# Kernel optimization log

Measured on AMD Instinct MI355X. Metric: run time of the kernel, lower is better.

## Reference

```python
import jax, jax.numpy as jnp
import numpy as np

B, L, D = 4, 2048, 768
K, M, CK = 12, 1, 4            # heads, thetas, conv kernel size
H = D // (K * M)               # 64
DIM_MEM = K * H                # 768
DIM_EXPAND = H * 3             # 192
DSH = DIM_EXPAND * 2           # 384 swiglu head dim
DST = K * DSH                  # 4608
DIM_FUSED = DIM_MEM + K + DST  # 5388
THETA_MIN, THETA_MAX = 1e-3, 3.0


def setup_inputs() -> dict:
    key = jax.random.key(0)
    ks = jax.random.split(key, 5)
    x = jax.random.normal(ks[0], (B, L, D), jnp.float32)
    W_in = jax.random.normal(ks[1], (D, DIM_FUSED), jnp.float32) * 0.02
    conv_w = jax.random.normal(ks[2], (CK, DIM_MEM + K), jnp.float32) * 0.2  # depthwise taps
    rms_scale = jnp.ones((H,), jnp.float32)
    # theta_raw init (M==1 branch): inverse-sigmoid of geomspace grid
    grid = np.geomspace(THETA_MIN, THETA_MAX, K).reshape(1, 1, K, 1, 1)
    base = np.tile(grid, (1, 1, 1, H, 1))
    u = np.clip((base - THETA_MIN) / (THETA_MAX - THETA_MIN), 1e-4, 1 - 1e-4)
    theta_raw = jnp.asarray(np.log(u) - np.log(1.0 - u), jnp.float32)
    decay_slopes = jnp.asarray(np.log(np.exp(np.geomspace(1e-3, 0.1, K)) - 1.0), jnp.float32)
    score_scale = jnp.ones((K,), jnp.float32)
    tanh_scale = jnp.ones((K,), jnp.float32)
    W_sw = jax.random.normal(ks[3], (2 * K * H * M, DST), jnp.float32) * 0.02
    W_out = jax.random.normal(ks[4], (K * DIM_EXPAND, D), jnp.float32) * 0.02
    return {"x": x, "W_in": W_in, "conv_w": conv_w, "rms_scale": rms_scale,
            "theta_raw": theta_raw, "decay_slopes": decay_slopes,
            "score_scale": score_scale, "tanh_scale": tanh_scale,
            "W_sw": W_sw, "W_out": W_out}


def reference(x, W_in, conv_w, rms_scale, theta_raw, decay_slopes,
              score_scale, tanh_scale, W_sw, W_out):
    # fused in-projection
    z_fused = jnp.einsum('bld,df->blf', x, W_in)
    z_mem = z_fused[..., :DIM_MEM + K]
    skip_direct = z_fused[..., DIM_MEM + K:]
    # causal depthwise conv (kernel size CK, left pad CK-1)
    zp = jnp.pad(z_mem, ((0, 0), (CK - 1, 0), (0, 0)))
    z_conv = sum(zp[:, j:j + L, :] * conv_w[j] for j in range(CK))
    z_mem = jax.nn.silu(z_conv)
    # memory keys + RMSNorm over H
    k_val = z_mem[..., :DIM_MEM].reshape(B, L, K, H)
    k_val = k_val * jax.lax.rsqrt(jnp.mean(k_val * k_val, axis=-1, keepdims=True) + 1e-6) * rms_scale
    s_raw = z_mem[..., DIM_MEM:]  # (B, L, K)
    # theta (M == 1)
    theta = THETA_MIN + (THETA_MAX - THETA_MIN) * jax.nn.sigmoid(theta_raw)  # (1,1,K,H,1)
    # decay time weights (num_anchor_heads == 0, maxlen == L)
    pos = jnp.arange(L, dtype=jnp.float32)
    slopes = jax.nn.softplus(decay_slopes).reshape(1, 1, K)
    dist = jnp.maximum(jnp.float32(L - 1) - pos, 0.0)
    log_time_weight = -slopes * dist[None, :, None]  # (1, L, K)
    log_p = jnp.clip(score_scale[None, None, :] * s_raw, -10.0, 10.0)
    p_w = jnp.exp(log_p + log_time_weight)  # (B, L, K)
    # characteristic-function encoding
    k5 = k_val[..., None]  # (B, L, K, H, 1)
    phi = jnp.tanh(k5 * tanh_scale.reshape(1, 1, K, 1, 1)) * theta
    kvw = k5 * p_w[..., None, None]
    re = kvw * jnp.cos(phi)
    im = kvw * jnp.sin(phi)
    # fused causal cumulative accumulation
    flat = K * H * M
    stack = jnp.concatenate([p_w, re.reshape(B, L, flat), im.reshape(B, L, flat)], axis=-1)
    cs = jnp.cumsum(stack, axis=1)
    den_acc = cs[..., :K]
    re_acc = cs[..., K:K + flat].reshape(B, L, K, H, M)
    im_acc = cs[..., K + flat:].reshape(B, L, K, H, M)
    inv_den = (1.0 / jnp.maximum(den_acc, 1e-4))[..., None, None]
    summary_flat = jnp.stack([re_acc * inv_den, im_acc * inv_den], axis=-1).reshape(B, L, -1)
    # SwiGLU with skip
    y_spectral = jnp.einsum('bls,sf->blf', summary_flat, W_sw).reshape(B, L, K, DSH)
    y_skip = skip_direct.reshape(B, L, K, DSH)
    y_spec_val, y_spec_gate = jnp.split(y_spectral, 2, axis=-1)
    y_skip_val, y_skip_gate = jnp.split(y_skip, 2, axis=-1)
    y_act = (y_spec_val + y_skip_val) * jax.nn.silu(y_spec_gate + y_skip_gate)
    out = jnp.einsum('blf,fd->bld', y_act.reshape(B, L, -1), W_out)
    return out
```

## Files before the change

### kernel.cpp

```cpp
#include <hip/hip_runtime.h>
#include <hip/hip_bf16.h>

#define B_       4
#define L_       2048
#define D_       768
#define K_       12
#define H_       64
#define CK_      4
#define DIM_MEM_ 768
#define DMK      780
#define NT       (B_*L_)
#define NSUM     1536
#define NACT     2304
#define NCHUNK   16
#define CHLEN    (L_/NCHUNK)
#define PSTRIDE  132

typedef __attribute__((ext_vector_type(8))) short          bf16x8;
typedef __attribute__((ext_vector_type(8))) unsigned short u16x8;
typedef __attribute__((ext_vector_type(4))) float          f32x4;

__device__ __forceinline__ ushort f2bf(float v) {
    __hip_bfloat16 h = __float2bfloat16(v);
    return *reinterpret_cast<ushort*>(&h);
}
__device__ __forceinline__ float tanh_fast(float x) {
    float t = __expf(-2.f * fabsf(x));
    float r = (1.f - t) / (1.f + t);
    return copysignf(r, x);
}

struct PrepJobs {
    const float* W[6];
    ushort*      out[6];
    int ldw[6], Kd[6], colbase[6], remap[6], ntx[6];
    int start[7];
    const float* cast_in;
    ushort*      cast_out;
    int n4;
};

__global__ __launch_bounds__(256)
void prep_all(PrepJobs J)
{
    int blk = blockIdx.x;
    if (blk >= J.start[6]) {
        int i = (blk - J.start[6]) * 256 + threadIdx.x;
        if (i < J.n4) {
            float4 v = reinterpret_cast<const float4*>(J.cast_in)[i];
            ushort4 o;
            o.x = f2bf(v.x); o.y = f2bf(v.y); o.z = f2bf(v.z); o.w = f2bf(v.w);
            reinterpret_cast<ushort4*>(J.cast_out)[i] = o;
        }
        return;
    }
    int j = 0;
    while (blk >= J.start[j + 1]) ++j;
    int rel = blk - J.start[j];
    int ntx = J.ntx[j];
    int n0 = (rel % ntx) * 32, k0 = (rel / ntx) * 32;
    const float* W = J.W[j];
    int ldw = J.ldw[j], Kd = J.Kd[j], colbase = J.colbase[j], remap = J.remap[j];
    ushort* out = J.out[j];

    __shared__ float tile[32][33];
    int tx = threadIdx.x & 31, ty = threadIdx.x >> 5;
    int n = n0 + tx;
    int c;
    if (remap) {
        int grp = n >> 5, which = (n >> 4) & 1, nn = (grp << 4) + (n & 15);
        c = colbase + (nn / 192) * 384 + which * 192 + (nn % 192);
    } else {
        c = colbase + n;
    }
    #pragma unroll
    for (int r = 0; r < 4; ++r)
        tile[ty + r*8][tx] = W[(size_t)(k0 + ty + r*8) * ldw + c];
    __syncthreads();
    #pragma unroll
    for (int r = 0; r < 4; ++r)
        out[(size_t)(n0 + ty + r*8) * Kd + k0 + tx] = f2bf(tile[tx][ty + r*8]);
}

__global__ __launch_bounds__(256)
void gemm_bf16_mfma(const ushort* __restrict__ A, const ushort* __restrict__ BT,
                    float* __restrict__ C, int Kd, int N, int ldc)
{
    __shared__ ushort As[128*64];
    __shared__ ushort Bs[128*64];
    int tid = threadIdx.x, lane = tid & 63;
    int lr = lane & 15, quad = lane >> 4;
    int wave = tid >> 6;
    int wr = (wave >> 1) * 64, wc = (wave & 1) * 64;
    int m0 = blockIdx.y * 128, n0 = blockIdx.x * 128;

    f32x4 acc[4][4] = {};

    int srow = tid >> 3;
    int tc   = tid & 7;
    const ushort* gA = A  + (size_t)(m0 + srow) * Kd + tc * 8;
    const ushort* gB = BT + (size_t)(n0 + srow) * Kd + tc * 8;
    int woff = srow * 64 + ((tc ^ (srow & 7)) * 8);
    int rx = lr & 7;

    for (int k0 = 0; k0 < Kd; k0 += 64) {
        u16x8 a[4], b[4];
        #pragma unroll
        for (int p = 0; p < 4; ++p) {
            a[p] = *reinterpret_cast<const u16x8*>(gA + (size_t)(32*p) * Kd);
            b[p] = *reinterpret_cast<const u16x8*>(gB + (size_t)(32*p) * Kd);
        }
        gA += 64; gB += 64;
        __syncthreads();
        #pragma unroll
        for (int p = 0; p < 4; ++p) {
            *reinterpret_cast<u16x8*>(As + woff + p*2048) = a[p];
            *reinterpret_cast<u16x8*>(Bs + woff + p*2048) = b[p];
        }
        __syncthreads();
        #pragma unroll
        for (int ks = 0; ks < 2; ++ks) {
            bf16x8 af[4], bf[4];
            #pragma unroll
            for (int i = 0; i < 4; ++i) {
                int ca = ((ks*4 + quad) ^ rx) * 8;
                af[i] = *reinterpret_cast<const bf16x8*>(As + (wr + i*16 + lr) * 64 + ca);
                bf[i] = *reinterpret_cast<const bf16x8*>(Bs + (wc + i*16 + lr) * 64 + ca);
            }
            #pragma unroll
            for (int i = 0; i < 4; ++i)
                #pragma unroll
                for (int j = 0; j < 4; ++j)
                    acc[i][j] = __builtin_amdgcn_mfma_f32_16x16x32_bf16(
                                    af[i], bf[j], acc[i][j], 0, 0, 0);
        }
    }

    #pragma unroll
    for (int i = 0; i < 4; ++i)
        #pragma unroll
        for (int j = 0; j < 4; ++j)
            #pragma unroll
            for (int r = 0; r < 4; ++r) {
                int row = m0 + wr + i*16 + quad*4 + r;
                int col = n0 + wc + j*16 + lr;
                if (col < N)
                    C[(size_t)row * ldc + col] = acc[i][j][r];
            }
}

#define G2NKT 36

#define GLOAD16(gp, dp) __builtin_amdgcn_global_load_lds( \
    (__attribute__((address_space(1))) const void*)(gp),  \
    (__attribute__((address_space(3))) void*)(dp), 16, 0, 0)

__device__ __forceinline__ void g2_stageA(ushort* lds_, int kt,
                                          const ushort* pAs, const ushort* pAx,
                                          int wave, int part)
{
    int ktc = kt > (G2NKT-1) ? (G2NKT-1) : kt;
    const ushort* g; size_t kd;
    if (ktc < 24) { g = pAs + ktc*64;      kd = 1536; }
    else          { g = pAx + (ktc-24)*64; kd = 768;  }
    g += (size_t)(part * 64) * kd;
    ushort* d = lds_ + (kt & 1) * 8192 + part * 4096 + wave * 512;
    GLOAD16(g,           d);
    GLOAD16(g + 32*kd,   d + 2048);
}

__device__ __forceinline__ void g2_stageB(ushort* lds_, int kt,
                                          const ushort* pBs, const ushort* pBx,
                                          int wave)
{
    int ktc = kt > (G2NKT-1) ? (G2NKT-1) : kt;
    const ushort* g; size_t kd;
    if (ktc < 24) { g = pBs + ktc*64;      kd = 1536; }
    else          { g = pBx + (ktc-24)*64; kd = 768;  }
    ushort* d = lds_ + 16384 + (kt & 1) * 12288 + wave * 512;
    #pragma unroll
    for (int s = 0; s < 6; ++s)
        GLOAD16(g + (size_t)(32*s)*kd, d + 2048*s);
}

__global__ __launch_bounds__(256, 2)
void gemm2_1ph(const ushort* __restrict__ Sm, const ushort* __restrict__ Xb,
               const ushort* __restrict__ WsC, const ushort* __restrict__ WiC,
               ushort* __restrict__ yact)
{
    __shared__ ushort lds[40960];
    const int tid  = threadIdx.x;
    const int lane = tid & 63, wave = tid >> 6;
    const int lr = lane & 15, quad = lane >> 4, rx = lr & 7;
    const int wr = (wave >> 1) * 64;
    const int wc = (wave & 1) * 96;
    const int m0 = blockIdx.y * 128, n0 = blockIdx.x * 192;

    const int sr = tid >> 3;
    const int sc = (tid & 7) ^ (sr & 7);
    const ushort* pAs = Sm  + (size_t)(m0 + sr) * 1536 + sc * 8;
    const ushort* pAx = Xb  + (size_t)(m0 + sr) * 768  + sc * 8;
    const ushort* pBs = WsC + (size_t)(n0 + sr) * 1536 + sc * 8;
    const ushort* pBx = WiC + (size_t)(n0 + sr) * 768  + sc * 8;

    f32x4 acc[4][6] = {};
    const int ca0 = (quad ^ rx) * 8;
    const int ca1 = ((4 + quad) ^ rx) * 8;

    g2_stageA(lds, 0, pAs, pAx, wave, 0);
    g2_stageA(lds, 0, pAs, pAx, wave, 1);
    g2_stageB(lds, 0, pBs, pBx, wave);
    asm volatile("s_waitcnt vmcnt(0)" ::: "memory");
    __builtin_amdgcn_s_barrier();

    #pragma unroll 1
    for (int g = 0; g < G2NKT; ++g) {
        const ushort* Ab = lds + (g & 1) * 8192;
        const ushort* Bb = lds + 16384 + (g & 1) * 12288;

        g2_stageA(lds, g + 1, pAs, pAx, wave, 0);
        g2_stageA(lds, g + 1, pAs, pAx, wave, 1);
        g2_stageB(lds, g + 1, pBs, pBx, wave);

        bf16x8 af[4][2], bfr[6][2];
        #pragma unroll
        for (int i = 0; i < 4; ++i) {
            const ushort* p = Ab + (wr + i*16 + lr) * 64;
            af[i][0] = *reinterpret_cast<const bf16x8*>(p + ca0);
            af[i][1] = *reinterpret_cast<const bf16x8*>(p + ca1);
        }
        #pragma unroll
        for (int j = 0; j < 6; ++j) {
            const ushort* p = Bb + (wc + j*16 + lr) * 64;
            bfr[j][0] = *reinterpret_cast<const bf16x8*>(p + ca0);
            bfr[j][1] = *reinterpret_cast<const bf16x8*>(p + ca1);
        }
        __builtin_amdgcn_s_setprio(1);
        #pragma unroll
        for (int ks = 0; ks < 2; ++ks)
            #pragma unroll
            for (int i = 0; i < 4; ++i)
                #pragma unroll
                for (int j = 0; j < 6; ++j)
                    acc[i][j] = __builtin_amdgcn_mfma_f32_16x16x32_bf16(
                                    af[i][ks], bfr[j][ks], acc[i][j], 0, 0, 0);
        __builtin_amdgcn_s_setprio(0);

        asm volatile("s_waitcnt vmcnt(0)" ::: "memory");
        __builtin_amdgcn_s_barrier();
    }

    const int vg0 = (n0 + wc) >> 5;
    #pragma unroll
    for (int i = 0; i < 4; ++i)
        #pragma unroll
        for (int p = 0; p < 3; ++p)
            #pragma unroll
            for (int r = 0; r < 4; ++r) {
                int row = m0 + wr + i*16 + quad*4 + r;
                int col = (vg0 + p)*16 + lr;
                float v  = acc[i][2*p][r];
                float gt = acc[i][2*p + 1][r];
                float y = v * (gt / (1.f + __expf(-gt)));
                yact[(size_t)row * NACT + col] = f2bf(y);
            }
}

__global__ __launch_bounds__(128)
void token_scan1(const float* __restrict__ zmem, const float* __restrict__ conv_w,
                 const float* __restrict__ rms_scale, const float* __restrict__ theta_raw,
                 const float* __restrict__ dslopes, const float* __restrict__ sscale,
                 const float* __restrict__ tscale,
                 float* __restrict__ reN, float* __restrict__ imN,
                 float* __restrict__ pwN, float* __restrict__ part)
{
    int blk = blockIdx.x;
    int chunk = blk & (NCHUNK - 1);
    int bk = blk >> 4;
    int k = bk % K_;
    int b = bk / K_;
    int tid = threadIdx.x;
    int h = tid & 63;
    int tt = tid >> 6;
    int l0 = chunk * CHLEN + tt * 64;

    int c  = k*H_ + h;
    int cs = DIM_MEM_ + k;

    float cw0 = conv_w[0*DMK + c], cw1 = conv_w[1*DMK + c];
    float cw2 = conv_w[2*DMK + c], cw3 = conv_w[3*DMK + c];
    float cs0 = conv_w[0*DMK + cs], cs1 = conv_w[1*DMK + cs];
    float cs2 = conv_w[2*DMK + cs], cs3 = conv_w[3*DMK + cs];
    float rs  = rms_scale[h];
    float th  = 0.001f + 2.999f * (1.f / (1.f + __expf(-theta_raw[c])));
    float ts  = tscale[k];
    float scl = sscale[k];
    float slope = log1pf(expf(dslopes[k]));

    const float* zb = zmem + (size_t)(b*L_) * DMK;

    float z3=0.f, z2=0.f, z1=0.f, s3=0.f, s2=0.f, s1=0.f;
    {
        int ll = l0 - 3;
        if (ll >= 0)     { z3 = zb[(size_t)ll*DMK + c];     s3 = zb[(size_t)ll*DMK + cs]; }
        if (ll + 1 >= 0) { z2 = zb[(size_t)(ll+1)*DMK + c]; s2 = zb[(size_t)(ll+1)*DMK + cs]; }
        if (ll + 2 >= 0) { z1 = zb[(size_t)(ll+2)*DMK + c]; s1 = zb[(size_t)(ll+2)*DMK + cs]; }
    }

    float sre = 0.f, sim = 0.f, spw = 0.f;
    size_t obase = (size_t)blk * (CHLEN*H_) + (size_t)(tt*64)*H_ + h;

    for (int i0 = 0; i0 < 64; i0 += 8) {
        float zl[8], sl[8];
        #pragma unroll
        for (int j = 0; j < 8; ++j) {
            int l = l0 + i0 + j;
            zl[j] = zb[(size_t)l*DMK + c];
            sl[j] = zb[(size_t)l*DMK + cs];
        }
        #pragma unroll
        for (int j = 0; j < 8; ++j) {
            int l = l0 + i0 + j;
            float a3 = zl[j], b3 = sl[j];
            float acc  = cw0*z3 + cw1*z2 + cw2*z1 + cw3*a3;
            float acc2 = cs0*s3 + cs1*s2 + cs2*s1 + cs3*b3;
            z3 = z2; z2 = z1; z1 = a3;
            s3 = s2; s2 = s1; s1 = b3;

            float kv = acc / (1.f + __expf(-acc));
            float ss = kv * kv;
            #pragma unroll
            for (int off = 32; off > 0; off >>= 1)
                ss += __shfl_xor(ss, off, 64);
            float kn  = kv * rsqrtf(ss * (1.f/64.f) + 1e-6f) * rs;
            float phi = tanh_fast(kn * ts) * th;

            float s  = acc2 / (1.f + expf(-acc2));
            float lp = fminf(10.f, fmaxf(-10.f, scl * s));
            float pwv = expf(lp - slope * (float)(L_ - 1 - l));

            float kvw = kn * pwv;
            float rev = kvw * __cosf(phi);
            float imv = kvw * __sinf(phi);
            reN[obase + (size_t)(i0 + j)*H_] = rev;
            imN[obase + (size_t)(i0 + j)*H_] = imv;
            sre += rev; sim += imv; spw += pwv;
            if (h == 0) pwN[(size_t)bk * L_ + l] = pwv;
        }
    }

    __shared__ float red[2][64], imd[2][64], pwd[2];
    red[tt][h] = sre; imd[tt][h] = sim;
    if (h == 0) pwd[tt] = spw;
    __syncthreads();
    size_t pb = (size_t)blk * PSTRIDE;
    if (tid < 64) part[pb + tid] = red[0][tid] + red[1][tid];
    else          part[pb + tid] = imd[0][tid - 64] + imd[1][tid - 64];
    if (tid == 0) part[pb + 128] = pwd[0] + pwd[1];
}

__global__ __launch_bounds__(128)
void scan_final2(const float* __restrict__ pwN, const float* __restrict__ reN,
                 const float* __restrict__ imN, const float* __restrict__ part,
                 ushort* __restrict__ summary)
{
    int blk = blockIdx.x;
    int chunk = blk & (NCHUNK - 1);
    int bk = blk >> 4;
    int k = bk % K_;
    int b = bk / K_;
    int tid = threadIdx.x;
    int h = tid & 63;
    int pi = tid >> 6;
    const float* __restrict__ src = pi ? imN : reN;
    int l0 = chunk * CHLEN;

    float acc = 0.f, dacc = 0.f;
    size_t pb0 = (size_t)(bk * NCHUNK) * PSTRIDE;
    for (int cn = 0; cn < chunk; ++cn) {
        acc  += part[pb0 + (size_t)cn*PSTRIDE + tid];
        dacc += part[pb0 + (size_t)cn*PSTRIDE + 128];
    }

    size_t base  = (size_t)blk * (CHLEN*H_) + h;
    size_t dbase = (size_t)bk * L_ + l0;
    int outch = 2*(k*H_ + h) + pi;
    for (int i0 = 0; i0 < CHLEN; i0 += 8) {
        float v[8], d[8];
        #pragma unroll
        for (int j = 0; j < 8; ++j) {
            v[j] = src[base + (size_t)(i0 + j)*H_];
            d[j] = pwN[dbase + i0 + j];
        }
        #pragma unroll
        for (int j = 0; j < 8; ++j) {
            acc += v[j]; dacc += d[j];
            float inv = 1.f / fmaxf(dacc, 1e-4f);
            summary[((size_t)(b*L_ + l0 + i0 + j))*NSUM + outch] = f2bf(acc * inv);
        }
    }
}

extern "C" void kernel_launch(void* const* d_in, const int* in_sizes, int n_in,
                              void* d_out, int out_size, void* d_ws, size_t ws_size,
                              hipStream_t stream)
{
    const float* x         = (const float*)d_in[0];
    const float* W_in      = (const float*)d_in[1];
    const float* conv_w    = (const float*)d_in[2];
    const float* rms_scale = (const float*)d_in[3];
    const float* theta_raw = (const float*)d_in[4];
    const float* dslopes   = (const float*)d_in[5];
    const float* sscale    = (const float*)d_in[6];
    const float* tscale    = (const float*)d_in[7];
    const float* W_sw      = (const float*)d_in[8];
    const float* W_out     = (const float*)d_in[9];
    float* out = (float*)d_out;
    char* ws   = (char*)d_ws;

    float*  zmem    = (float*) (ws + 0);
    ushort* summary = (ushort*)(ws + 0);
    float*  pw      = (float*) (ws + 25559040);
    float*  re      = (float*) (ws + 25952256);
    float*  im      = (float*) (ws + 51118080);
    ushort* yact    = (ushort*)(ws + 25952256);
    float*  part    = (float*) (ws + 76283904);
    ushort* xb      = (ushort*)(ws + 76689408);
    ushort* WiCat   = (ushort*)(ws + 89272320);
    ushort* WsCat   = (ushort*)(ws + 96350208);
    ushort* WoT     = (ushort*)(ws + 110505984);
    ushort* WimT    = (ushort*)(ws + 114044928);

    PrepJobs J{};
    J.W[0]=W_in;  J.out[0]=WiCat; J.ldw[0]=5388; J.Kd[0]=768;  J.colbase[0]=780; J.remap[0]=1; J.ntx[0]=144;
    J.W[1]=W_sw;  J.out[1]=WsCat; J.ldw[1]=4608; J.Kd[1]=1536; J.colbase[1]=0;   J.remap[1]=1; J.ntx[1]=144;
    J.W[2]=W_out; J.out[2]=WoT;   J.ldw[2]=768;  J.Kd[2]=2304; J.colbase[2]=0;   J.remap[2]=0; J.ntx[2]=24;
    J.W[3]=W_in;  J.out[3]=WimT;  J.ldw[3]=5388; J.Kd[3]=768;  J.colbase[3]=0;   J.remap[3]=0; J.ntx[3]=28;
    int tiles[4] = {144*24, 144*48, 24*72, 28*24};
    J.start[0] = 0;
    for (int j = 0; j < 4; ++j) J.start[j+1] = J.start[j] + tiles[j];
    J.start[5] = J.start[4];
    J.start[6] = J.start[4];
    J.cast_in = x; J.cast_out = xb; J.n4 = NT*D_/4;
    int nblk = J.start[6] + (J.n4 + 255)/256;

    dim3 blk(256);
    prep_all<<<dim3(nblk), blk, 0, stream>>>(J);
    gemm_bf16_mfma<<<dim3(7, 64), blk, 0, stream>>>(xb, WimT, zmem, 768, 780, 780);
    token_scan1<<<dim3(B_*K_*NCHUNK), dim3(128), 0, stream>>>(
        zmem, conv_w, rms_scale, theta_raw, dslopes, sscale, tscale,
        re, im, pw, part);
    scan_final2<<<dim3(B_*K_*NCHUNK), dim3(128), 0, stream>>>(pw, re, im, part, summary);
    gemm2_1ph<<<dim3(24, 64), dim3(256), 0, stream>>>(summary, xb, WsCat, WiCat, yact);
    gemm_bf16_mfma<<<dim3(6, 64), blk, 0, stream>>>(yact, WoT, out, 2304, 768, 768);
}
```

Measured before the change: 399.3 us.

## Double-buffer GEMM tiles with direct global-to-LDS loads in first and last GEMMs

Replaces the register-staged single-buffer bf16 MFMA GEMM with a version that uses global_load_lds to copy tiles straight into a double-buffered LDS region. The next K-tile is prefetched while the current one is used, with one barrier per iteration instead of two. All fragments for a tile are loaded up front, and s_setprio raises wave priority around the MFMA block. The kernel doubles its LDS use (64KB) and adds launch bounds for two blocks per CU, which could limit occupancy.

```diff
diff --git a/kernel.cpp b/kernel.cpp
--- a/kernel.cpp
+++ b/kernel.cpp
@@ -82,58 +82,78 @@
         out[(size_t)(n0 + ty + r*8) * Kd + k0 + tx] = f2bf(tile[tx][ty + r*8]);
 }
 
-__global__ __launch_bounds__(256)
-void gemm_bf16_mfma(const ushort* __restrict__ A, const ushort* __restrict__ BT,
-                    float* __restrict__ C, int Kd, int N, int ldc)
-{
-    __shared__ ushort As[128*64];
-    __shared__ ushort Bs[128*64];
-    int tid = threadIdx.x, lane = tid & 63;
-    int lr = lane & 15, quad = lane >> 4;
-    int wave = tid >> 6;
-    int wr = (wave >> 1) * 64, wc = (wave & 1) * 64;
-    int m0 = blockIdx.y * 128, n0 = blockIdx.x * 128;
+#define GLOAD16(gp, dp) __builtin_amdgcn_global_load_lds( \
+    (__attribute__((address_space(1))) const void*)(gp),  \
+    (__attribute__((address_space(3))) void*)(dp), 16, 0, 0)
+
+__device__ __forceinline__ void g13_stage(ushort* dst, const ushort* src, int kd)
+{
+    #pragma unroll
+    for (int s = 0; s < 4; ++s)
+        GLOAD16(src + (size_t)(32*s)*kd, dst + 2048*s);
+}
+
+__global__ __launch_bounds__(256, 2)
+void gemm13_1ph(const ushort* __restrict__ A, const ushort* __restrict__ BT,
+                float* __restrict__ C, int Kd, int N, int ldc)
+{
+    __shared__ ushort lds[32768];
+    const int tid  = threadIdx.x;
+    const int lane = tid & 63, wave = tid >> 6;
+    const int lr = lane & 15, quad = lane >> 4, rx = lr & 7;
+    const int wr = (wave >> 1) * 64, wc = (wave & 1) * 64;
+    const int m0 = blockIdx.y * 128, n0 = blockIdx.x * 128;
+    const int NKT = Kd >> 6;
+
+    const int sr = tid >> 3;
+    const int sc = (tid & 7) ^ (sr & 7);
+    const ushort* pA = A  + (size_t)(m0 + sr) * Kd + sc * 8;
+    const ushort* pB = BT + (size_t)(n0 + sr) * Kd + sc * 8;
 
     f32x4 acc[4][4] = {};
-
-    int srow = tid >> 3;
-    int tc   = tid & 7;
-    const ushort* gA = A  + (size_t)(m0 + srow) * Kd + tc * 8;
-    const ushort* gB = BT + (size_t)(n0 + srow) * Kd + tc * 8;
-    int woff = srow * 64 + ((tc ^ (srow & 7)) * 8);
-    int rx = lr & 7;
-
-    for (int k0 = 0; k0 < Kd; k0 += 64) {
-        u16x8 a[4], b[4];
-        #pragma unroll
-        for (int p = 0; p < 4; ++p) {
-            a[p] = *reinterpret_cast<const u16x8*>(gA + (size_t)(32*p) * Kd);
-            b[p] = *reinterpret_cast<const u16x8*>(gB + (size_t)(32*p) * Kd);
-        }
-        gA += 64; gB += 64;
-        __syncthreads();
-        #pragma unroll
-        for (int p = 0; p < 4; ++p) {
-            *reinterpret_cast<u16x8*>(As + woff + p*2048) = a[p];
-            *reinterpret_cast<u16x8*>(Bs + woff + p*2048) = b[p];
-        }
-        __syncthreads();
-        #pragma unroll
-        for (int ks = 0; ks < 2; ++ks) {
-            bf16x8 af[4], bf[4];
-            #pragma unroll
-            for (int i = 0; i < 4; ++i) {
-                int ca = ((ks*4 + quad) ^ rx) * 8;
-                af[i] = *reinterpret_cast<const bf16x8*>(As + (wr + i*16 + lr) * 64 + ca);
-                bf[i] = *reinterpret_cast<const bf16x8*>(Bs + (wc + i*16 + lr) * 64 + ca);
-            }
+    const int ca0 = (quad ^ rx) * 8;
+    const int ca1 = ((4 + quad) ^ rx) * 8;
+
+    g13_stage(lds + wave*512,         pA, Kd);
+    g13_stage(lds + 16384 + wave*512, pB, Kd);
+    asm volatile("s_waitcnt vmcnt(0)" ::: "memory");
+    __builtin_amdgcn_s_barrier();
+
+    #pragma unroll 1
+    for (int g = 0; g < NKT; ++g) {
+        const ushort* Ab = lds + (g & 1) * 8192;
+        const ushort* Bb = lds + 16384 + (g & 1) * 8192;
+
+        int nk = (g + 1 < NKT) ? g + 1 : NKT - 1;
+        g13_stage(lds + ((g + 1) & 1) * 8192 + wave*512,         pA + nk*64, Kd);
+        g13_stage(lds + 16384 + ((g + 1) & 1) * 8192 + wave*512, pB + nk*64, Kd);
+
+        bf16x8 af[4][2], bf[4][2];
+        #pragma unroll
+        for (int i = 0; i < 4; ++i) {
+            const ushort* p = Ab + (wr + i*16 + lr) * 64;
+            af[i][0] = *reinterpret_cast<const bf16x8*>(p + ca0);
+            af[i][1] = *reinterpret_cast<const bf16x8*>(p + ca1);
+        }
+        #pragma unroll
+        for (int j = 0; j < 4; ++j) {
+            const ushort* p = Bb + (wc + j*16 + lr) * 64;
+            bf[j][0] = *reinterpret_cast<const bf16x8*>(p + ca0);
+            bf[j][1] = *reinterpret_cast<const bf16x8*>(p + ca1);
+        }
+        __builtin_amdgcn_s_setprio(1);
+        #pragma unroll
+        for (int ks = 0; ks < 2; ++ks)
             #pragma unroll
             for (int i = 0; i < 4; ++i)
                 #pragma unroll
                 for (int j = 0; j < 4; ++j)
                     acc[i][j] = __builtin_amdgcn_mfma_f32_16x16x32_bf16(
-                                    af[i], bf[j], acc[i][j], 0, 0, 0);
-        }
+                                    af[i][ks], bf[j][ks], acc[i][j], 0, 0, 0);
+        __builtin_amdgcn_s_setprio(0);
+
+        asm volatile("s_waitcnt vmcnt(0)" ::: "memory");
+        __builtin_amdgcn_s_barrier();
     }
 
     #pragma unroll
@@ -150,10 +170,6 @@
 }
 
 #define G2NKT 36
-
-#define GLOAD16(gp, dp) __builtin_amdgcn_global_load_lds( \
-    (__attribute__((address_space(1))) const void*)(gp),  \
-    (__attribute__((address_space(3))) void*)(dp), 16, 0, 0)
 
 __device__ __forceinline__ void g2_stageA(ushort* lds_, int kt,
                                           const ushort* pAs, const ushort* pAx,
@@ -446,11 +462,11 @@
 
     dim3 blk(256);
     prep_all<<<dim3(nblk), blk, 0, stream>>>(J);
-    gemm_bf16_mfma<<<dim3(7, 64), blk, 0, stream>>>(xb, WimT, zmem, 768, 780, 780);
+    gemm13_1ph<<<dim3(7, 64), blk, 0, stream>>>(xb, WimT, zmem, 768, 780, 780);
     token_scan1<<<dim3(B_*K_*NCHUNK), dim3(128), 0, stream>>>(
         zmem, conv_w, rms_scale, theta_raw, dslopes, sscale, tscale,
         re, im, pw, part);
     scan_final2<<<dim3(B_*K_*NCHUNK), dim3(128), 0, stream>>>(pw, re, im, part, summary);
     gemm2_1ph<<<dim3(24, 64), dim3(256), 0, stream>>>(summary, xb, WsCat, WiCat, yact);
-    gemm_bf16_mfma<<<dim3(6, 64), blk, 0, stream>>>(yact, WoT, out, 2304, 768, 768);
-}
+    gemm13_1ph<<<dim3(6, 64), blk, 0, stream>>>(yact, WoT, out, 2304, 768, 768);
+}
```

New measurement: 394.6 us. No clear change (-1.2%).
